# Performance work log

Hardware: AMD Instinct MI355X
Metric: run time of the kernel (lower is better)

The kernel has to match this reference:

```python
import jax, jax.numpy as jnp
import numpy as np

N_ENC, B, T, D_ENC = 3, 256, 168, 32
U, H, D_DEC, D_EXT = 256, 24, 1, 16


def _gru_cell(x, h, W, Uw, b):
    # Keras-style GRU cell: gates ordered [z, r, n]; h' = (1-z)*h + z*n
    u = Uw.shape[0]
    xg = x @ W + b            # [B, 3U]
    hg = h @ Uw               # [B, 3U]
    z = jax.nn.sigmoid(xg[:, :u] + hg[:, :u])
    r = jax.nn.sigmoid(xg[:, u:2 * u] + hg[:, u:2 * u])
    n = jnp.tanh(xg[:, 2 * u:] + r * hg[:, 2 * u:])
    return (1.0 - z) * h + z * n


def _run_gru(x, W, Uw, b):
    # x: [B, T, D] -> outputs [B, T, U], last state [B, U]
    h0 = jnp.zeros((x.shape[0], Uw.shape[0]), x.dtype)

    def step(h, xt):
        h2 = _gru_cell(xt, h, W, Uw, b)
        return h2, h2

    hT, ys = jax.lax.scan(step, h0, jnp.swapaxes(x, 0, 1))
    return jnp.swapaxes(ys, 0, 1), hT


def setup_inputs() -> dict:
    key = jax.random.key(0)
    ks = jax.random.split(key, 18)
    s = 0.05
    d_in_dec = N_ENC * U + D_DEC
    d_state = U + N_ENC * U
    return {
        "enc_inputs": jax.random.normal(ks[0], (N_ENC, B, T, D_ENC), jnp.float32),
        "dec_input": jax.random.normal(ks[1], (B, H, D_DEC), jnp.float32),
        "ext_feat": jax.random.normal(ks[2], (B, H, D_EXT), jnp.float32),
        "enc_W": jax.random.normal(ks[3], (N_ENC, D_ENC, 3 * U), jnp.float32) * s,
        "enc_U": jax.random.normal(ks[4], (N_ENC, U, 3 * U), jnp.float32) * s,
        "enc_b": jnp.zeros((N_ENC, 3 * U), jnp.float32),
        "att_W1": jax.random.normal(ks[5], (N_ENC, U, U), jnp.float32) * s,
        "att_W2": jax.random.normal(ks[6], (N_ENC, U, U), jnp.float32) * s,
        "att_v": jax.random.normal(ks[7], (N_ENC, U), jnp.float32) * s,
        "dec_W": jax.random.normal(ks[8], (d_in_dec, 3 * U), jnp.float32) * s,
        "dec_U": jax.random.normal(ks[9], (U, 3 * U), jnp.float32) * s,
        "dec_b": jnp.zeros((3 * U,), jnp.float32),
        "ext_W": jax.random.normal(ks[10], (D_EXT, U), jnp.float32) * s,
        "ext_b": jnp.zeros((U,), jnp.float32),
        "out1_W": jax.random.normal(ks[11], (d_state + U, U), jnp.float32) * s,
        "out1_b": jnp.zeros((U,), jnp.float32),
        "out2_W": jax.random.normal(ks[12], (U, D_DEC), jnp.float32) * s,
        "out2_b": jnp.zeros((D_DEC,), jnp.float32),
    }


def reference(enc_inputs, dec_input, ext_feat, enc_W, enc_U, enc_b,
              att_W1, att_W2, att_v, dec_W, dec_U, dec_b,
              ext_W, ext_b, out1_W, out1_b, out2_W, out2_b):
    b = dec_input.shape[0]
    horizon = dec_input.shape[1]

    # ---- encoders (vmapped GRU over the n_enc streams) ----
    enc_out, _ = jax.vmap(_run_gru)(enc_inputs, enc_W, enc_U, enc_b)  # [n,B,T,U]
    # Precompute Bahdanau keys once: W1 @ enc_outputs
    enc_proj = jnp.einsum('nbtu,nuv->nbtv', enc_out, att_W1)          # [n,B,T,U]

    h0 = jnp.zeros((b, U), dec_input.dtype)
    c0 = jnp.zeros((b, N_ENC * U), dec_input.dtype)

    def dec_step(carry, d_t):
        h, c = carry
        x_t = jnp.concatenate([c, d_t], axis=-1)                      # [B, n*U + D_dec]
        h = _gru_cell(x_t, h, dec_W, dec_U, dec_b)                    # [B, U]
        # Bahdanau attention per encoder, query = decoder state
        q = jnp.einsum('bu,nuv->nbv', h, att_W2)                      # [n,B,U]
        score = jnp.einsum('nbtv,nv->nbt',
                           jnp.tanh(enc_proj + q[:, :, None, :]), att_v)
        alpha = jax.nn.softmax(score, axis=-1)                        # [n,B,T]
        ctx = jnp.einsum('nbt,nbtu->nbu', alpha, enc_out)             # [n,B,U]
        c = jnp.transpose(ctx, (1, 0, 2)).reshape(b, N_ENC * U)
        return (h, c), h

    (h_last, c_last), _ = jax.lax.scan(dec_step, (h0, c0),
                                       jnp.swapaxes(dec_input, 0, 1))

    # ---- output head ----
    state = jnp.concatenate([h_last, c_last], axis=-1)                # [B, U + n*U]
    ed = jnp.broadcast_to(state[:, None, :], (b, horizon, state.shape[-1]))
    ext = jax.nn.relu(ext_feat @ ext_W + ext_b)                       # [B, H, U]
    x = jnp.concatenate([ed, ext], axis=-1)
    x = jax.nn.relu(x @ out1_W + out1_b)
    return x @ out2_W + out2_b                                        # [B, H, target_dim]
```

## Files before the change

kernel.cpp:

```cpp
#include <hip/hip_runtime.h>
#include <math.h>

typedef unsigned short u16;
typedef float f4v __attribute__((ext_vector_type(4)));
typedef _Float16 hfv8 __attribute__((ext_vector_type(8)));

#define MFMAH(a,b,c) __builtin_amdgcn_mfma_f32_16x16x32_f16((a),(b),(c),0,0,0)

__device__ __forceinline__ float bf2f(u16 x){
    unsigned int u = ((unsigned int)x) << 16;
    float f; __builtin_memcpy(&f, &u, 4); return f;
}
__device__ __forceinline__ u16 f2bf(float f){
    unsigned int u; __builtin_memcpy(&u, &f, 4);
    u += 0x7fffu + ((u >> 16) & 1u);
    return (u16)(u >> 16);
}
__device__ __forceinline__ u16 f2h(float f){
    _Float16 h = (_Float16)f;
    u16 b; __builtin_memcpy(&b, &h, 2); return b;
}
__device__ __forceinline__ float h2f(u16 b){
    _Float16 h; __builtin_memcpy(&h, &b, 2); return (float)h;
}
__device__ __forceinline__ float ldmix(const void* p, long i, int mode){
    if (mode) return ((const float*)p)[i];
    return bf2f(((const u16*)p)[i]);
}
__device__ __forceinline__ float frcp(float x){ return __builtin_amdgcn_rcpf(x); }
__device__ __forceinline__ float sigf(float x){ return frcp(1.0f+__expf(-x)); }
__device__ __forceinline__ float tanh_fast(float x){
    float e = __expf(2.0f*x);
    return 1.0f - 2.0f*frcp(1.0f+e);
}

#define BATCH 256
#define TLEN 168
#define HOR 24

#define OFF_FLAG 0ull
#define OFF_SENT 16ull
#define OFF_WF   256ull
#define OFF_UP   8721920ull
#define OFF_WP   9901568ull
#define OFF_DWP  10049024ull
#define OFF_DUP  11228672ull
#define OFF_H0   11621888ull
#define OFF_H1   11884032ull
#define OFF_C    12146176ull
#define OFF_W1P  12932608ull
#define OFF_SP   13719040ull
#define OFF_E    13981184ull
#define OFF_PACK0 OFF_E
#define OFF_PACK1 (OFF_E + 524288ull)
#define OFF_ENCOUT 17126912ull
#define OFF_PROJ 83187200ull
#define OFF_W2P  116217344ull
#define NEED_BYTES 149247488ull

#define W_ENCW 0
#define W_ENCU 73728
#define W_ENCB 663552
#define W_AW1  665856
#define W_AW2  862464
#define W_AV   1059072
#define W_DECW 1059840
#define W_DECU 1650432
#define W_DECB 1847040
#define W_EXTW 1847808
#define W_EXTB 1851904
#define W_O1W  1852160
#define W_O1B  2179840
#define W_O2W  2180096
#define W_O2B  2180352

__device__ const int c_wsz[15]  = {73728,589824,2304,196608,196608,768,590592,196608,768,4096,256,327680,256,256,1};
__device__ const int c_woff[15] = {W_ENCW,W_ENCU,W_ENCB,W_AW1,W_AW2,W_AV,W_DECW,W_DECU,W_DECB,W_EXTW,W_EXTB,W_O1W,W_O1B,W_O2W,W_O2B};

struct P15 { const void* p[15]; };

#define SENT_MAGIC 0x5AFE0000u
__device__ __forceinline__ void put_sent(char* ws, int idx){
    ((unsigned int*)(ws+OFF_SENT))[idx] = SENT_MAGIC | (unsigned int)idx;
}

__global__ __launch_bounds__(256) void k_probe(const u16* w16, char* ws)
{
    __shared__ float red[256];
    int tid = threadIdx.x;
    float mb = 0.0f;
    for (int i = tid; i < 2048; i += 256){
        float a = fabsf(bf2f(w16[i]));
        if (a > mb) mb = a;
    }
    red[tid] = mb;
    __syncthreads();
    if (tid == 0){
        for (int i = 1; i < 256; ++i) if (red[i] > mb) mb = red[i];
        *(int*)(ws+OFF_FLAG) = (mb > 1000.0f) ? 1 : 0;
        put_sent(ws, 0);
    }
}

__global__ __launch_bounds__(256) void k_convert(P15 in, char* ws)
{
    int mode = *(const int*)(ws+OFF_FLAG);
    float* F = (float*)(ws+OFF_WF);
    int y = blockIdx.y;
    int sz = c_wsz[y], off = c_woff[y];
    for (long i = (long)blockIdx.x*256 + threadIdx.x; i < sz; i += 256L*256L)
        F[off + i] = ldmix(in.p[y], i, mode);
    if (blockIdx.x==0 && blockIdx.y==0 && threadIdx.x==0) put_sent(ws, 1);
}

__global__ __launch_bounds__(64) void k_pack(char* ws)
{
    const float* F = (const float*)(ws+OFF_WF);
    int m = blockIdx.y;
    if (m >= 11){
        const float* s = F + W_AW2 + (m-11)*65536;
        u16* d = (u16*)(ws+OFF_W2P) + (m-11)*65536;
        int i = blockIdx.x*64 + threadIdx.x;
        if (i < 65536){
            int k = i>>8, u = i&255;
            d[(k>>1)*512 + u*2 + (k&1)] = f2h(s[i]);
        }
        return;
    }
    const float* src; u16* dst; int K, N; int duo = 0;
    switch (m) {
      case 0: case 1: case 2:
        src = F + W_ENCU + m*196608; dst = (u16*)(ws+OFF_UP) + m*196608; K=256; N=768; break;
      case 3: case 4: case 5:
        src = F + W_ENCW + (m-3)*24576; dst = (u16*)(ws+OFF_WP) + (m-3)*24576; K=32; N=768; break;
      case 6:
        src = F + W_DECW; dst = (u16*)(ws+OFF_DWP); K=768; N=768; break;
      case 7:
        src = F + W_DECU; dst = (u16*)(ws+OFF_DUP); K=256; N=768; break;
      default:
        src = F + W_AW1 + (m-8)*65536; dst = (u16*)(ws+OFF_W1P) + (m-8)*131072; K=256; N=256; duo=1; break;
    }
    int KT = K>>5, NT = N>>4;
    int tau = blockIdx.x;
    if (tau < KT*NT){
        int ct = tau / KT, kt = tau % KT;
        int l = threadIdx.x, q = l>>4, c = l&15;
        #pragma unroll
        for (int j = 0; j < 8; ++j){
            float v = src[(size_t)(kt*32 + q*8 + j)*N + ct*16 + c];
            u16 hi = f2h(v);
            size_t di = ((size_t)(ct*KT+kt)*64 + l)*8 + j;
            dst[di] = hi;
            if (duo) dst[65536 + di] = f2h(v - h2f(hi));
        }
    }
    if (blockIdx.x==0 && blockIdx.y==0 && threadIdx.x==0) put_sent(ws, 6);
}

__global__ __launch_bounds__(256) void k_init(char* ws)
{
    long idx = (long)blockIdx.x*256 + threadIdx.x;
    if (idx < 65536) ((float*)(ws+OFF_H0))[idx] = 0.0f;
    else if (idx < 262144) ((float*)(ws+OFF_C))[idx-65536] = 0.0f;
    else if (idx < 393216) ((int*)(ws+OFF_PACK0))[idx-262144] = 0;
}

__global__ __launch_bounds__(512, 2) void k_enc(const void* __restrict__ enc_in,
                                                char* __restrict__ ws,
                                                u16* __restrict__ enc_out)
{
    const float* __restrict__ F = (const float*)(ws+OFF_WF);
    int mode = *(const int*)(ws+OFF_FLAG);
    const int n  = blockIdx.y;
    const int b0 = blockIdx.x*16;
    const int tid = threadIdx.x;
    const int w = tid>>6, l = tid&63, quad = l>>4, c15 = l&15;

    __shared__ __align__(16) u16 hA[2][8][64][8];
    __shared__ __align__(16) u16 sx[2][64][8];
    __shared__ __align__(16) u16 nU[128][64][8];

    const u16* __restrict__ upn = (const u16*)(ws+OFF_UP) + n*196608;
    const u16* __restrict__ wpn = (const u16*)(ws+OFF_WP) + n*24576;

    {
        const uint4* s4 = (const uint4*)(upn + 131072);
        uint4* d4 = (uint4*)&nU[0][0][0];
        for (int i = tid; i < 8192; i += 512) d4[i] = s4[i];
    }
    {
        int* z0 = (int*)&hA[0][0][0][0];
        for (int i = tid; i < 2048; i += 512) z0[i]=0;
    }
    float h[8];
    #pragma unroll
    for (int i=0;i<8;++i) h[i]=0.0f;

    float bzr[2], brr[2], bnr[2];
    #pragma unroll
    for (int si=0;si<2;++si){
        int u = (w*2+si)*16 + c15;
        bzr[si] = F[W_ENCB + n*768 + u];
        brr[si] = F[W_ENCB + n*768 + 256 + u];
        bnr[si] = F[W_ENCB + n*768 + 512 + u];
    }

    hfv8 Bz[2][8], Br[2][8];
    #pragma unroll
    for (int si=0;si<2;++si){
        int ct = w*2+si;
        #pragma unroll
        for (int kt=0;kt<8;++kt){
            Bz[si][kt] = *(const hfv8*)(upn + ((size_t)(ct*8+kt)*64 + l)*8);
            Br[si][kt] = *(const hfv8*)(upn + ((size_t)((16+ct)*8+kt)*64 + l)*8);
        }
    }
    #pragma unroll
    for (int si=0;si<2;++si)
        #pragma unroll
        for (int kt=0;kt<8;++kt)
            asm volatile("" : "+v"(Bz[si][kt]), "+v"(Br[si][kt]));

    const int mm = tid>>5, kk2 = tid&31;
    sx[0][(kk2>>3)*16 + mm][kk2&7] =
        f2h(ldmix(enc_in, (((long)(n*BATCH + b0 + mm))*TLEN + 0)*32 + kk2, mode));
    __syncthreads();

    for (int t = 0; t < TLEN; ++t){
        int p = t & 1;

        int tt = (t+1 < TLEN) ? (t+1) : t;
        float xr = ldmix(enc_in, (((long)(n*BATCH + b0 + mm))*TLEN + tt)*32 + kk2, mode);

        hfv8 ah[8];
        #pragma unroll
        for (int kt=0; kt<8; ++kt)
            ah[kt] = *(const hfv8*)&hA[p][kt][l][0];
        hfv8 ax = *(const hfv8*)&sx[p][l][0];

        #pragma unroll
        for (int si=0; si<2; ++si){
            int ct = w*2 + si;
            f4v az  = {0.f,0.f,0.f,0.f};
            f4v ar  = {0.f,0.f,0.f,0.f};
            f4v anx = {0.f,0.f,0.f,0.f};
            f4v anh = {0.f,0.f,0.f,0.f};
            az  = MFMAH(ax, *(const hfv8*)(wpn + ((size_t)ct*64 + l)*8), az);
            ar  = MFMAH(ax, *(const hfv8*)(wpn + ((size_t)(16+ct)*64 + l)*8), ar);
            anx = MFMAH(ax, *(const hfv8*)(wpn + ((size_t)(32+ct)*64 + l)*8), anx);
            #pragma unroll
            for (int kt=0; kt<8; ++kt) az = MFMAH(ah[kt], Bz[si][kt], az);
            #pragma unroll
            for (int kt=0; kt<8; ++kt) ar = MFMAH(ah[kt], Br[si][kt], ar);
            #pragma unroll
            for (int kt=0; kt<8; ++kt)
                anh = MFMAH(ah[kt], *(const hfv8*)&nU[ct*8+kt][l][0], anh);
            int u = ct*16 + c15;
            #pragma unroll
            for (int j=0;j<4;++j){
                int m = quad*4 + j;
                float z = sigf(az[j] + bzr[si]);
                float r = sigf(ar[j] + brr[si]);
                float ng = tanh_fast(anx[j] + bnr[si] + r*anh[j]);
                float hn = (1.0f - z)*h[si*4+j] + z*ng;
                h[si*4+j] = hn;
                int kt = u>>5, q2 = (u>>3)&3, j2 = u&7;
                hA[1-p][kt][q2*16+m][j2] = f2h(hn);
            }
        }
        sx[1-p][(kk2>>3)*16 + mm][kk2&7] = f2h(xr);
        __syncthreads();
        {
            int c = tid & 31, m2 = tid >> 5;
            *reinterpret_cast<uint4*>(enc_out + (((long)(n*BATCH + b0 + m2))*TLEN + t)*256 + c*8) =
                *(const uint4*)&hA[1-p][c>>2][(c&3)*16 + m2][0];
        }
    }
    if (blockIdx.x==0 && blockIdx.y==0 && tid==0) put_sent(ws, 2);
}

__global__ __launch_bounds__(256) void k_projm(char* __restrict__ ws)
{
    const u16* __restrict__ enc16 = (const u16*)(ws+OFF_ENCOUT);
    const u16* __restrict__ w1p = (const u16*)(ws+OFF_W1P);
    u16* __restrict__ proj = (u16*)(ws+OFF_PROJ);
    const int n = blockIdx.y;
    const long r0 = (long)blockIdx.x*64;
    const int tid = threadIdx.x;
    const int w = tid>>6, l = tid&63, quad = l>>4, c15 = l&15;

    __shared__ __align__(16) u16 ob[64][264];

    const u16* erow = enc16 + ((long)n*43008 + r0 + w*16 + c15)*256;
    hfv8 a[8];
    #pragma unroll
    for (int kt=0; kt<8; ++kt)
        a[kt] = *(const hfv8*)(erow + kt*32 + quad*8);

    const u16* wb = w1p + (long)n*131072;
    #pragma unroll
    for (int ct=0; ct<16; ++ct){
        f4v acc = {0.f,0.f,0.f,0.f};
        #pragma unroll
        for (int kt=0; kt<8; ++kt)
            acc = MFMAH(a[kt], *(const hfv8*)(wb + ((size_t)(ct*8+kt)*64 + l)*8), acc);
        #pragma unroll
        for (int kt=0; kt<8; ++kt)
            acc = MFMAH(a[kt], *(const hfv8*)(wb + 65536 + ((size_t)(ct*8+kt)*64 + l)*8), acc);
        #pragma unroll
        for (int j=0;j<4;++j)
            ob[w*16 + quad*4 + j][ct*16 + c15] = f2h(acc[j]);
    }
    __syncthreads();
    for (int i = tid; i < 2048; i += 256){
        int r = i>>5, c = i&31;
        *reinterpret_cast<uint4*>(proj + ((long)n*43008 + r0 + r)*256 + c*8) =
            *(const uint4*)&ob[r][c*8];
    }
    if (blockIdx.x==0 && blockIdx.y==0 && tid==0) put_sent(ws, 3);
}

__global__ __launch_bounds__(192) void k_dec_gru(
    char* __restrict__ ws, const float* __restrict__ h_in, float* __restrict__ h_out,
    const u16* __restrict__ packC, u16* __restrict__ packN,
    const void* __restrict__ dec_in, int step)
{
    const float* __restrict__ F = (const float*)(ws+OFF_WF);
    int mode = *(const int*)(ws+OFF_FLAG);
    const u16* __restrict__ dwp = (const u16*)(ws+OFF_DWP);
    const u16* __restrict__ dup = (const u16*)(ws+OFF_DUP);
    const int bx = blockIdx.x;
    const int b0 = bx*16;
    const int us = blockIdx.y;
    const int u0 = us*16;
    const int tid = threadIdx.x;
    const int gate = tid>>6, l = tid&63, quad = l>>4, c15 = l&15;
    const int ct = gate*16 + us;

    __shared__ float gz[16][16], gr[16][16], gx[16][16], gh[16][16];

    const u16* pA = packC + (size_t)bx*16384;

    f4v accA  = {0.f,0.f,0.f,0.f};
    f4v accA2 = {0.f,0.f,0.f,0.f};
    f4v accB  = {0.f,0.f,0.f,0.f};
    f4v accB2 = {0.f,0.f,0.f,0.f};

    #pragma unroll
    for (int kg = 0; kg < 32; ++kg){
        hfv8 av = *(const hfv8*)(pA + ((size_t)kg*64 + l)*8);
        const u16* bp = (kg < 24) ? dwp + ((size_t)(ct*24 + kg)*64 + l)*8
                                  : dup + ((size_t)(ct*8  + (kg-24))*64 + l)*8;
        hfv8 bv = *(const hfv8*)bp;
        if (gate == 2 && kg >= 24){
            if (kg & 1) accB2 = MFMAH(av, bv, accB2);
            else        accB  = MFMAH(av, bv, accB);
        } else {
            if (kg & 1) accA2 = MFMAH(av, bv, accA2);
            else        accA  = MFMAH(av, bv, accA);
        }
    }
    accA = accA + accA2;
    accB = accB + accB2;

    #pragma unroll
    for (int j=0;j<4;++j){
        int m = quad*4 + j;
        if (gate == 0) gz[m][c15] = accA[j];
        else if (gate == 1) gr[m][c15] = accA[j];
        else { gx[m][c15] = accA[j]; gh[m][c15] = accB[j]; }
    }
    __syncthreads();
    for (int e = tid; e < 256; e += 192){
        int m = e>>4, j = e&15;
        int u = u0 + j;
        int b = b0 + m;
        float db = ldmix(dec_in, (long)b*HOR + step, mode);
        float sz = gz[m][j] + db*F[W_DECW + 768*768 + u]       + F[W_DECB + u];
        float sr = gr[m][j] + db*F[W_DECW + 768*768 + 256 + u] + F[W_DECB + 256 + u];
        float sn = gx[m][j] + db*F[W_DECW + 768*768 + 512 + u] + F[W_DECB + 512 + u];
        float z = sigf(sz);
        float r = sigf(sr);
        float ng = tanh_fast(sn + r*gh[m][j]);
        float hn = (1.0f - z)*h_in[(long)b*256 + u] + z*ng;
        h_out[(long)b*256 + u] = hn;
        int kk = u & 31;
        int kg = 24 + (u >> 5);
        packN[(((size_t)bx*32 + kg)*64 + (kk>>3)*16 + m)*8 + (kk&7)] = f2h(hn);
    }
}

__global__ __launch_bounds__(256) void k_attn(char* __restrict__ ws,
                                              const float* __restrict__ hvec,
                                              u16* __restrict__ packN)
{
    const float* __restrict__ F = (const float*)(ws+OFF_WF);
    const u16* __restrict__ proj = (const u16*)(ws+OFF_PROJ);
    const u16* __restrict__ enc16 = (const u16*)(ws+OFF_ENCOUT);
    float* __restrict__ C = (float*)(ws+OFF_C);
    const int b = blockIdx.x, n = blockIdx.y;
    const int tid = threadIdx.x;
    const int w = tid>>6, l = tid&63;

    __shared__ float ps[TLEN][65];
    __shared__ float sc[TLEN];
    __shared__ float red[8];
    __shared__ float hrow[256];
    __shared__ float sq[256];

    hrow[tid] = hvec[(long)b*256 + tid];
    __syncthreads();
    {
        const u16* W2p = (const u16*)(ws+OFF_W2P) + n*65536;
        float q0=0.f,q1=0.f,q2=0.f,q3=0.f;
        #pragma unroll 4
        for (int k2 = 0; k2 < 128; k2 += 2){
            unsigned va = *(const unsigned*)(W2p + (size_t)k2*512 + tid*2);
            unsigned vb = *(const unsigned*)(W2p + (size_t)(k2+1)*512 + tid*2);
            q0 += hrow[2*k2  ]*h2f((u16)(va & 0xffffu));
            q1 += hrow[2*k2+1]*h2f((u16)(va >> 16));
            q2 += hrow[2*k2+2]*h2f((u16)(vb & 0xffffu));
            q3 += hrow[2*k2+3]*h2f((u16)(vb >> 16));
        }
        sq[tid] = (q0+q1)+(q2+q3);
    }
    __syncthreads();

    float qv[4], vv[4];
    #pragma unroll
    for (int c4 = 0; c4 < 4; ++c4){
        qv[c4] = sq[c4*64 + l];
        vv[c4] = F[W_AV + n*256 + c4*64 + l];
    }
    long base = ((long)n*43008 + (long)b*TLEN)*256;
    const u16* pb = proj + base;

    for (int i = 0; i < 42; ++i){
        int t = w*42 + i;
        float s = 0.0f;
        #pragma unroll
        for (int c4 = 0; c4 < 4; ++c4){
            float pv = h2f(pb[(long)t*256 + c4*64 + l]);
            s += vv[c4]*tanh_fast(pv + qv[c4]);
        }
        ps[t][l] = s;
    }
    __syncthreads();

    float sval = 0.0f;
    if (tid < TLEN){
        float s0=0.f,s1=0.f,s2=0.f,s3=0.f,s4=0.f,s5=0.f,s6=0.f,s7=0.f;
        #pragma unroll
        for (int j = 0; j < 64; j += 8){
            s0 += ps[tid][j];   s1 += ps[tid][j+1];
            s2 += ps[tid][j+2]; s3 += ps[tid][j+3];
            s4 += ps[tid][j+4]; s5 += ps[tid][j+5];
            s6 += ps[tid][j+6]; s7 += ps[tid][j+7];
        }
        sval = ((s0+s1)+(s2+s3)) + ((s4+s5)+(s6+s7));
    }

    float m = (tid < TLEN) ? sval : -1e30f;
    #pragma unroll
    for (int off = 32; off > 0; off >>= 1) m = fmaxf(m, __shfl_xor(m, off, 64));
    if (l == 0) red[w] = m;
    __syncthreads();
    float mx = fmaxf(fmaxf(red[0],red[1]), fmaxf(red[2],red[3]));

    float ex = 0.0f;
    if (tid < TLEN){ ex = __expf(sval - mx); sc[tid] = ex; }
    float su = ex;
    #pragma unroll
    for (int off = 32; off > 0; off >>= 1) su += __shfl_xor(su, off, 64);
    if (l == 0) red[4+w] = su;
    __syncthreads();
    float inv = frcp((red[4]+red[5]) + (red[6]+red[7]));

    const u16* eb = enc16 + base;
    float a0=0.f,a1=0.f,a2=0.f,a3=0.f,a4=0.f,a5=0.f,a6=0.f,a7=0.f;
    for (int t = 0; t < TLEN; t += 8){
        a0 += sc[t  ]*h2f(eb[(long)(t  )*256 + tid]);
        a1 += sc[t+1]*h2f(eb[(long)(t+1)*256 + tid]);
        a2 += sc[t+2]*h2f(eb[(long)(t+2)*256 + tid]);
        a3 += sc[t+3]*h2f(eb[(long)(t+3)*256 + tid]);
        a4 += sc[t+4]*h2f(eb[(long)(t+4)*256 + tid]);
        a5 += sc[t+5]*h2f(eb[(long)(t+5)*256 + tid]);
        a6 += sc[t+6]*h2f(eb[(long)(t+6)*256 + tid]);
        a7 += sc[t+7]*h2f(eb[(long)(t+7)*256 + tid]);
    }
    float cv = (((a0+a1)+(a2+a3)) + ((a4+a5)+(a6+a7)))*inv;
    C[(long)b*768 + n*256 + tid] = cv;
    {
        int kg = n*8 + (tid>>5), kk = tid&31;
        packN[(((size_t)(b>>4)*32 + kg)*64 + (kk>>3)*16 + (b&15))*8 + (kk&7)] = f2h(cv);
    }
    if (b==0 && n==0 && tid==0) put_sent(ws, 4);
}

__global__ __launch_bounds__(256) void k_head1(char* ws, const float* h_last)
{
    const float* F = (const float*)(ws+OFF_WF);
    const float* C = (const float*)(ws+OFF_C);
    float* SP = (float*)(ws+OFF_SP);
    const int b0 = blockIdx.x*8;
    const int tid = threadIdx.x;

    __shared__ float A[8][1024];
    for (int i = tid; i < 8192; i += 256){
        int r = i >> 10, k = i & 1023;
        A[r][k] = (k < 256) ? h_last[(long)(b0+r)*256 + k]
                            : C[(long)(b0+r)*768 + (k-256)];
    }
    __syncthreads();

    const float* W = F + W_O1W;
    float acc[8];
    float bc = F[W_O1B + tid];
    #pragma unroll
    for (int r = 0; r < 8; ++r) acc[r] = bc;
    for (int k = 0; k < 1024; ++k){
        float w = W[k*256 + tid];
        #pragma unroll
        for (int r = 0; r < 8; ++r) acc[r] += A[r][k]*w;
    }
    for (int r = 0; r < 8; ++r)
        SP[(long)(b0+r)*256 + tid] = acc[r];
}

__global__ __launch_bounds__(256) void k_ext(const void* ext_feat, char* ws)
{
    const float* F = (const float*)(ws+OFF_WF);
    u16* E = (u16*)(ws+OFF_E);
    int mode = *(const int*)(ws+OFF_FLAG);
    const int r0 = blockIdx.x*64;
    const int tid = threadIdx.x;
    __shared__ float ef[64][16];
    for (int i = tid; i < 1024; i += 256)
        ef[i>>4][i&15] = ldmix(ext_feat, (long)(r0 + (i>>4))*16 + (i&15), mode);
    float wreg[16];
    #pragma unroll
    for (int k = 0; k < 16; ++k) wreg[k] = F[W_EXTW + k*256 + tid];
    float bb = F[W_EXTB + tid];
    __syncthreads();
    for (int r = 0; r < 64; ++r){
        float a = bb;
        #pragma unroll
        for (int k = 0; k < 16; ++k) a += ef[r][k]*wreg[k];
        E[(long)(r0+r)*256 + tid] = f2bf((a > 0.0f) ? a : 0.0f);
    }
}

__global__ __launch_bounds__(256) void k_head2(char* ws, void* out)
{
    const float* F = (const float*)(ws+OFF_WF);
    const u16* E = (const u16*)(ws+OFF_E);
    const float* SP = (const float*)(ws+OFF_SP);
    int mode = *(const int*)(ws+OFF_FLAG);
    const int r0 = blockIdx.x*16;
    const int tid = threadIdx.x;
    const int w = tid>>6, l = tid&63;

    __shared__ float A[16][256];
    __shared__ float x1[16][257];
    for (int i = tid; i < 4096; i += 256)
        A[i>>8][i&255] = bf2f(E[(long)r0*256 + i]);
    __syncthreads();

    const float* W = F + W_O1W + 1024*256;
    float acc[16];
    float bc = F[W_O1B + tid];
    #pragma unroll
    for (int r = 0; r < 16; ++r) acc[r] = 0.0f;
    for (int k = 0; k < 256; ++k){
        float wv = W[k*256 + tid];
        #pragma unroll
        for (int r = 0; r < 16; ++r) acc[r] += A[r][k]*wv;
    }
    for (int r = 0; r < 16; ++r){
        int g = r0 + r;
        int b = g / HOR;
        float v = acc[r] + SP[(long)b*256 + tid] + bc;
        x1[r][tid] = (v > 0.0f) ? v : 0.0f;
    }
    __syncthreads();

    float w2v[4];
    #pragma unroll
    for (int c4 = 0; c4 < 4; ++c4) w2v[c4] = F[W_O2W + c4*64 + l];
    float b2 = F[W_O2B];
    #pragma unroll
    for (int rr = 0; rr < 4; ++rr){
        int m = w*4 + rr;
        float s = 0.0f;
        #pragma unroll
        for (int c4 = 0; c4 < 4; ++c4) s += x1[m][c4*64 + l]*w2v[c4];
        for (int off = 32; off > 0; off >>= 1) s += __shfl_xor(s, off, 64);
        if (l == 0){
            float val = s + b2;
            long g = r0 + m;
            if (mode == 0) ((u16*)out)[g] = f2bf(val);
            else           ((float*)out)[g] = val;
        }
    }
    if (blockIdx.x==0 && tid==0) put_sent(ws, 5);
}

__global__ __launch_bounds__(64) void MTANet_7593502179851_kernel(char* ws, void* out)
{
    if (threadIdx.x == 0){
        const unsigned int* sent = (const unsigned int*)(ws+OFF_SENT);
        int mode = *(const int*)(ws+OFF_FLAG);
        for (int i = 0; i < 7; ++i){
            if (sent[i] != (SENT_MAGIC | (unsigned int)i)){
                float code = 400.0f + 10.0f*(float)i;
                if (mode == 0) ((u16*)out)[0] = f2bf(code);
                else           ((float*)out)[0] = code;
                break;
            }
        }
    }
}

__global__ __launch_bounds__(64) void k_diag(void* out, float code)
{
    if (threadIdx.x == 0){
        ((u16*)out)[0] = f2bf(code);
        ((float*)out)[1] = code;
    }
}

extern "C" void kernel_launch(void* const* d_in, const int* in_sizes, int n_in,
                              void* d_out, int out_size, void* d_ws, size_t ws_size,
                              hipStream_t stream)
{
    char* ws = (char*)d_ws;

    static const int exp_sizes[18] = {
        4128768, 6144, 98304, 73728, 589824, 2304, 196608, 196608, 768,
        590592, 196608, 768, 4096, 256, 327680, 256, 256, 1 };
    int bad_i = -1;
    if (n_in != 18) bad_i = 99;
    else for (int i = 0; i < 18; ++i)
        if (in_sizes[i] != exp_sizes[i]){ bad_i = i; break; }
    if (bad_i >= 0){
        k_diag<<<dim3(1), dim3(64), 0, stream>>>(d_out, 900.0f + (float)bad_i);
        return;
    }
    if (ws_size < (size_t)NEED_BYTES){
        k_diag<<<dim3(1), dim3(64), 0, stream>>>(d_out, 600.0f);
        return;
    }

    P15 wp;
    for (int i = 0; i < 15; ++i) wp.p[i] = d_in[3+i];

    hipError_t le[12];
    for (int i = 0; i < 12; ++i) le[i] = hipSuccess;
    (void)hipGetLastError();
    #define CHK(slot) { hipError_t e_ = hipGetLastError(); if (e_ != hipSuccess && le[slot] == hipSuccess) le[slot] = e_; }

    k_probe<<<dim3(1), dim3(256), 0, stream>>>((const u16*)d_in[3], ws);       CHK(0)
    k_convert<<<dim3(256,15), dim3(256), 0, stream>>>(wp, ws);                 CHK(1)
    k_pack<<<dim3(1152,14), dim3(64), 0, stream>>>(ws);                        CHK(2)
    k_init<<<dim3(1536), dim3(256), 0, stream>>>(ws);                          CHK(3)
    k_enc<<<dim3(16,3), dim3(512), 0, stream>>>(d_in[0], ws, (u16*)(ws+OFF_ENCOUT)); CHK(4)
    k_projm<<<dim3(672,3), dim3(256), 0, stream>>>(ws);                        CHK(5)

    float* hbuf0 = (float*)(ws+OFF_H0);
    float* hbuf1 = (float*)(ws+OFF_H1);
    u16* pk0 = (u16*)(ws+OFF_PACK0);
    u16* pk1 = (u16*)(ws+OFF_PACK1);
    float* h_last = hbuf0;
    for (int s = 0; s < HOR; ++s){
        float* h_in  = (s & 1) ? hbuf1 : hbuf0;
        float* h_out = (s & 1) ? hbuf0 : hbuf1;
        u16* pc = (s & 1) ? pk1 : pk0;
        u16* pn = (s & 1) ? pk0 : pk1;
        k_dec_gru<<<dim3(16,16), dim3(192), 0, stream>>>(ws, h_in, h_out, pc, pn, d_in[1], s); CHK(6)
        k_attn<<<dim3(256,3), dim3(256), 0, stream>>>(ws, h_out, pn);           CHK(7)
        h_last = h_out;
    }
    k_head1<<<dim3(32), dim3(256), 0, stream>>>(ws, h_last);                   CHK(8)
    k_ext<<<dim3(96), dim3(256), 0, stream>>>(d_in[2], ws);                    CHK(9)
    k_head2<<<dim3(384), dim3(256), 0, stream>>>(ws, d_out);                   CHK(10)
    MTANet_7593502179851_kernel<<<dim3(1), dim3(64), 0, stream>>>(ws, d_out);
    #undef CHK

    for (int i = 0; i < 12; ++i){
        if (le[i] != hipSuccess){
            k_diag<<<dim3(1), dim3(64), 0, stream>>>(d_out, 800.0f + (float)i);
            break;
        }
    }
}
```

Before: 1.648 ms.

## Fuse decoder GRU and attention steps into one persistent kernel with group barriers

Replaces the 48 per-step launches (GRU kernel plus attention kernel for each of 24 horizon steps) with a single persistent kernel of 256 blocks. Each group of 16 blocks synchronizes through global atomic counters, used as spin barriers, after the GRU update and after attention. Attention now loops over the three encoders inside a block and splits the query and context reductions across 512 threads. The W2 packed buffer moves to a smaller offset. This removes launch overhead, at the cost of depending on all 256 blocks being co-resident and on spin-wait correctness.

```diff
diff --git a/kernel.cpp b/kernel.cpp
--- a/kernel.cpp
+++ b/kernel.cpp
@@ -40,6 +40,7 @@
 
 #define OFF_FLAG 0ull
 #define OFF_SENT 16ull
+#define OFF_CNT  128ull
 #define OFF_WF   256ull
 #define OFF_UP   8721920ull
 #define OFF_WP   9901568ull
@@ -53,9 +54,9 @@
 #define OFF_E    13981184ull
 #define OFF_PACK0 OFF_E
 #define OFF_PACK1 (OFF_E + 524288ull)
+#define OFF_W2P   (OFF_E + 1048576ull)
 #define OFF_ENCOUT 17126912ull
 #define OFF_PROJ 83187200ull
-#define OFF_W2P  116217344ull
 #define NEED_BYTES 149247488ull
 
 #define W_ENCW 0
@@ -163,6 +164,7 @@
     if (idx < 65536) ((float*)(ws+OFF_H0))[idx] = 0.0f;
     else if (idx < 262144) ((float*)(ws+OFF_C))[idx-65536] = 0.0f;
     else if (idx < 393216) ((int*)(ws+OFF_PACK0))[idx-262144] = 0;
+    if (idx < 32) ((unsigned*)(ws+OFF_CNT))[idx] = 0u;
 }
 
 __global__ __launch_bounds__(512, 2) void k_enc(const void* __restrict__ enc_in,
@@ -228,7 +230,6 @@
 
     for (int t = 0; t < TLEN; ++t){
         int p = t & 1;
-
         int tt = (t+1 < TLEN) ? (t+1) : t;
         float xr = ldmix(enc_in, (((long)(n*BATCH + b0 + mm))*TLEN + tt)*32 + kk2, mode);
 
@@ -320,181 +321,219 @@
     if (blockIdx.x==0 && blockIdx.y==0 && tid==0) put_sent(ws, 3);
 }
 
-__global__ __launch_bounds__(192) void k_dec_gru(
-    char* __restrict__ ws, const float* __restrict__ h_in, float* __restrict__ h_out,
-    const u16* __restrict__ packC, u16* __restrict__ packN,
-    const void* __restrict__ dec_in, int step)
+__global__ __launch_bounds__(512, 2) void k_dec_all(
+    char* __restrict__ ws, const void* __restrict__ dec_in,
+    u16* __restrict__ pk0, u16* __restrict__ pk1,
+    float* __restrict__ h0, float* __restrict__ h1)
 {
     const float* __restrict__ F = (const float*)(ws+OFF_WF);
-    int mode = *(const int*)(ws+OFF_FLAG);
     const u16* __restrict__ dwp = (const u16*)(ws+OFF_DWP);
     const u16* __restrict__ dup = (const u16*)(ws+OFF_DUP);
-    const int bx = blockIdx.x;
-    const int b0 = bx*16;
-    const int us = blockIdx.y;
-    const int u0 = us*16;
-    const int tid = threadIdx.x;
-    const int gate = tid>>6, l = tid&63, quad = l>>4, c15 = l&15;
-    const int ct = gate*16 + us;
-
-    __shared__ float gz[16][16], gr[16][16], gx[16][16], gh[16][16];
-
-    const u16* pA = packC + (size_t)bx*16384;
-
-    f4v accA  = {0.f,0.f,0.f,0.f};
-    f4v accA2 = {0.f,0.f,0.f,0.f};
-    f4v accB  = {0.f,0.f,0.f,0.f};
-    f4v accB2 = {0.f,0.f,0.f,0.f};
-
-    #pragma unroll
-    for (int kg = 0; kg < 32; ++kg){
-        hfv8 av = *(const hfv8*)(pA + ((size_t)kg*64 + l)*8);
-        const u16* bp = (kg < 24) ? dwp + ((size_t)(ct*24 + kg)*64 + l)*8
-                                  : dup + ((size_t)(ct*8  + (kg-24))*64 + l)*8;
-        hfv8 bv = *(const hfv8*)bp;
-        if (gate == 2 && kg >= 24){
-            if (kg & 1) accB2 = MFMAH(av, bv, accB2);
-            else        accB  = MFMAH(av, bv, accB);
-        } else {
-            if (kg & 1) accA2 = MFMAH(av, bv, accA2);
-            else        accA  = MFMAH(av, bv, accA);
-        }
-    }
-    accA = accA + accA2;
-    accB = accB + accB2;
-
-    #pragma unroll
-    for (int j=0;j<4;++j){
-        int m = quad*4 + j;
-        if (gate == 0) gz[m][c15] = accA[j];
-        else if (gate == 1) gr[m][c15] = accA[j];
-        else { gx[m][c15] = accA[j]; gh[m][c15] = accB[j]; }
-    }
-    __syncthreads();
-    for (int e = tid; e < 256; e += 192){
-        int m = e>>4, j = e&15;
-        int u = u0 + j;
-        int b = b0 + m;
-        float db = ldmix(dec_in, (long)b*HOR + step, mode);
-        float sz = gz[m][j] + db*F[W_DECW + 768*768 + u]       + F[W_DECB + u];
-        float sr = gr[m][j] + db*F[W_DECW + 768*768 + 256 + u] + F[W_DECB + 256 + u];
-        float sn = gx[m][j] + db*F[W_DECW + 768*768 + 512 + u] + F[W_DECB + 512 + u];
-        float z = sigf(sz);
-        float r = sigf(sr);
-        float ng = tanh_fast(sn + r*gh[m][j]);
-        float hn = (1.0f - z)*h_in[(long)b*256 + u] + z*ng;
-        h_out[(long)b*256 + u] = hn;
-        int kk = u & 31;
-        int kg = 24 + (u >> 5);
-        packN[(((size_t)bx*32 + kg)*64 + (kk>>3)*16 + m)*8 + (kk&7)] = f2h(hn);
-    }
-}
-
-__global__ __launch_bounds__(256) void k_attn(char* __restrict__ ws,
-                                              const float* __restrict__ hvec,
-                                              u16* __restrict__ packN)
-{
-    const float* __restrict__ F = (const float*)(ws+OFF_WF);
     const u16* __restrict__ proj = (const u16*)(ws+OFF_PROJ);
     const u16* __restrict__ enc16 = (const u16*)(ws+OFF_ENCOUT);
     float* __restrict__ C = (float*)(ws+OFF_C);
-    const int b = blockIdx.x, n = blockIdx.y;
+    int mode = *(const int*)(ws+OFF_FLAG);
+
+    const int blk = blockIdx.x;
+    const int g = blk >> 4;
+    const int r = blk & 15;
     const int tid = threadIdx.x;
     const int w = tid>>6, l = tid&63;
-
+    const int b = g*16 + r;
+
+    unsigned* cnt = (unsigned*)(ws+OFF_CNT) + (size_t)g*2;
+
+    __shared__ float gz[16][16], gr[16][16], gx[16][16], gh[16][16];
     __shared__ float ps[TLEN][65];
     __shared__ float sc[TLEN];
-    __shared__ float red[8];
+    __shared__ float red[16];
     __shared__ float hrow[256];
     __shared__ float sq[256];
-
-    hrow[tid] = hvec[(long)b*256 + tid];
-    __syncthreads();
-    {
-        const u16* W2p = (const u16*)(ws+OFF_W2P) + n*65536;
-        float q0=0.f,q1=0.f,q2=0.f,q3=0.f;
-        #pragma unroll 4
-        for (int k2 = 0; k2 < 128; k2 += 2){
-            unsigned va = *(const unsigned*)(W2p + (size_t)k2*512 + tid*2);
-            unsigned vb = *(const unsigned*)(W2p + (size_t)(k2+1)*512 + tid*2);
-            q0 += hrow[2*k2  ]*h2f((u16)(va & 0xffffu));
-            q1 += hrow[2*k2+1]*h2f((u16)(va >> 16));
-            q2 += hrow[2*k2+2]*h2f((u16)(vb & 0xffffu));
-            q3 += hrow[2*k2+3]*h2f((u16)(vb >> 16));
-        }
-        sq[tid] = (q0+q1)+(q2+q3);
-    }
-    __syncthreads();
-
-    float qv[4], vv[4];
-    #pragma unroll
-    for (int c4 = 0; c4 < 4; ++c4){
-        qv[c4] = sq[c4*64 + l];
-        vv[c4] = F[W_AV + n*256 + c4*64 + l];
-    }
-    long base = ((long)n*43008 + (long)b*TLEN)*256;
-    const u16* pb = proj + base;
-
-    for (int i = 0; i < 42; ++i){
-        int t = w*42 + i;
-        float s = 0.0f;
-        #pragma unroll
-        for (int c4 = 0; c4 < 4; ++c4){
-            float pv = h2f(pb[(long)t*256 + c4*64 + l]);
-            s += vv[c4]*tanh_fast(pv + qv[c4]);
-        }
-        ps[t][l] = s;
-    }
-    __syncthreads();
-
-    float sval = 0.0f;
-    if (tid < TLEN){
-        float s0=0.f,s1=0.f,s2=0.f,s3=0.f,s4=0.f,s5=0.f,s6=0.f,s7=0.f;
-        #pragma unroll
-        for (int j = 0; j < 64; j += 8){
-            s0 += ps[tid][j];   s1 += ps[tid][j+1];
-            s2 += ps[tid][j+2]; s3 += ps[tid][j+3];
-            s4 += ps[tid][j+4]; s5 += ps[tid][j+5];
-            s6 += ps[tid][j+6]; s7 += ps[tid][j+7];
-        }
-        sval = ((s0+s1)+(s2+s3)) + ((s4+s5)+(s6+s7));
-    }
-
-    float m = (tid < TLEN) ? sval : -1e30f;
-    #pragma unroll
-    for (int off = 32; off > 0; off >>= 1) m = fmaxf(m, __shfl_xor(m, off, 64));
-    if (l == 0) red[w] = m;
-    __syncthreads();
-    float mx = fmaxf(fmaxf(red[0],red[1]), fmaxf(red[2],red[3]));
-
-    float ex = 0.0f;
-    if (tid < TLEN){ ex = __expf(sval - mx); sc[tid] = ex; }
-    float su = ex;
-    #pragma unroll
-    for (int off = 32; off > 0; off >>= 1) su += __shfl_xor(su, off, 64);
-    if (l == 0) red[4+w] = su;
-    __syncthreads();
-    float inv = frcp((red[4]+red[5]) + (red[6]+red[7]));
-
-    const u16* eb = enc16 + base;
-    float a0=0.f,a1=0.f,a2=0.f,a3=0.f,a4=0.f,a5=0.f,a6=0.f,a7=0.f;
-    for (int t = 0; t < TLEN; t += 8){
-        a0 += sc[t  ]*h2f(eb[(long)(t  )*256 + tid]);
-        a1 += sc[t+1]*h2f(eb[(long)(t+1)*256 + tid]);
-        a2 += sc[t+2]*h2f(eb[(long)(t+2)*256 + tid]);
-        a3 += sc[t+3]*h2f(eb[(long)(t+3)*256 + tid]);
-        a4 += sc[t+4]*h2f(eb[(long)(t+4)*256 + tid]);
-        a5 += sc[t+5]*h2f(eb[(long)(t+5)*256 + tid]);
-        a6 += sc[t+6]*h2f(eb[(long)(t+6)*256 + tid]);
-        a7 += sc[t+7]*h2f(eb[(long)(t+7)*256 + tid]);
-    }
-    float cv = (((a0+a1)+(a2+a3)) + ((a4+a5)+(a6+a7)))*inv;
-    C[(long)b*768 + n*256 + tid] = cv;
-    {
-        int kg = n*8 + (tid>>5), kk = tid&31;
-        packN[(((size_t)(b>>4)*32 + kg)*64 + (kk>>3)*16 + (b&15))*8 + (kk&7)] = f2h(cv);
-    }
-    if (b==0 && n==0 && tid==0) put_sent(ws, 4);
+    __shared__ float sqp[2][256];
+    __shared__ float ctxp[2][256];
+
+    for (int s = 0; s < HOR; ++s){
+        const u16* packC = (s & 1) ? pk1 : pk0;
+        u16* packN      = (s & 1) ? pk0 : pk1;
+        const float* h_in  = (s & 1) ? h1 : h0;
+        float* h_out       = (s & 1) ? h0 : h1;
+
+        if (tid < 192){
+            const int gate = tid>>6, quad = l>>4, c15 = l&15;
+            const int ct = gate*16 + r;
+            const u16* pA = packC + (size_t)g*16384;
+
+            f4v accA  = {0.f,0.f,0.f,0.f};
+            f4v accA2 = {0.f,0.f,0.f,0.f};
+            f4v accB  = {0.f,0.f,0.f,0.f};
+            f4v accB2 = {0.f,0.f,0.f,0.f};
+            #pragma unroll
+            for (int kg = 0; kg < 32; ++kg){
+                hfv8 av = *(const hfv8*)(pA + ((size_t)kg*64 + l)*8);
+                const u16* bp = (kg < 24) ? dwp + ((size_t)(ct*24 + kg)*64 + l)*8
+                                          : dup + ((size_t)(ct*8  + (kg-24))*64 + l)*8;
+                hfv8 bv = *(const hfv8*)bp;
+                if (gate == 2 && kg >= 24){
+                    if (kg & 1) accB2 = MFMAH(av, bv, accB2);
+                    else        accB  = MFMAH(av, bv, accB);
+                } else {
+                    if (kg & 1) accA2 = MFMAH(av, bv, accA2);
+                    else        accA  = MFMAH(av, bv, accA);
+                }
+            }
+            accA = accA + accA2;
+            accB = accB + accB2;
+            #pragma unroll
+            for (int j=0;j<4;++j){
+                int m = quad*4 + j;
+                if (gate == 0) gz[m][c15] = accA[j];
+                else if (gate == 1) gr[m][c15] = accA[j];
+                else { gx[m][c15] = accA[j]; gh[m][c15] = accB[j]; }
+            }
+        }
+        __syncthreads();
+        if (tid < 256){
+            int m = tid>>4, j = tid&15;
+            int u = r*16 + j;
+            int bb = g*16 + m;
+            float db = ldmix(dec_in, (long)bb*HOR + s, mode);
+            float sz = gz[m][j] + db*F[W_DECW + 768*768 + u]       + F[W_DECB + u];
+            float sr = gr[m][j] + db*F[W_DECW + 768*768 + 256 + u] + F[W_DECB + 256 + u];
+            float sn = gx[m][j] + db*F[W_DECW + 768*768 + 512 + u] + F[W_DECB + 512 + u];
+            float z = sigf(sz);
+            float rr2 = sigf(sr);
+            float ng = tanh_fast(sn + rr2*gh[m][j]);
+            float hn = (1.0f - z)*h_in[(long)bb*256 + u] + z*ng;
+            h_out[(long)bb*256 + u] = hn;
+            int kk = u & 31;
+            int kg = 24 + (u >> 5);
+            packN[(((size_t)g*32 + kg)*64 + (kk>>3)*16 + m)*8 + (kk&7)] = f2h(hn);
+        }
+
+        __syncthreads();
+        if (tid == 0){
+            __threadfence();
+            atomicAdd(cnt+0, 1u);
+            unsigned tgt = 16u*(unsigned)(s+1);
+            int sp = 0;
+            while (atomicAdd(cnt+0, 0u) < tgt && sp < 4000000) ++sp;
+        }
+        __syncthreads();
+        __threadfence();
+
+        if (tid < 256) hrow[tid] = h_out[(long)b*256 + tid];
+        __syncthreads();
+
+        for (int n = 0; n < 3; ++n){
+            {
+                const u16* W2p = (const u16*)(ws+OFF_W2P) + n*65536;
+                int uu = tid & 255, half = tid >> 8;
+                float q0=0.f,q1=0.f,q2=0.f,q3=0.f;
+                #pragma unroll 4
+                for (int k2 = half*64; k2 < half*64+64; k2 += 2){
+                    unsigned va = *(const unsigned*)(W2p + (size_t)k2*512 + uu*2);
+                    unsigned vb = *(const unsigned*)(W2p + (size_t)(k2+1)*512 + uu*2);
+                    q0 += hrow[2*k2  ]*h2f((u16)(va & 0xffffu));
+                    q1 += hrow[2*k2+1]*h2f((u16)(va >> 16));
+                    q2 += hrow[2*k2+2]*h2f((u16)(vb & 0xffffu));
+                    q3 += hrow[2*k2+3]*h2f((u16)(vb >> 16));
+                }
+                sqp[half][uu] = (q0+q1)+(q2+q3);
+            }
+            __syncthreads();
+            if (tid < 256) sq[tid] = sqp[0][tid] + sqp[1][tid];
+            __syncthreads();
+
+            float qv[4], vv[4];
+            #pragma unroll
+            for (int c4 = 0; c4 < 4; ++c4){
+                qv[c4] = sq[c4*64 + l];
+                vv[c4] = F[W_AV + n*256 + c4*64 + l];
+            }
+            long base = ((long)n*43008 + (long)b*TLEN)*256;
+            const u16* pb = proj + base;
+
+            for (int i = 0; i < 21; ++i){
+                int t = w*21 + i;
+                float sacc = 0.0f;
+                #pragma unroll
+                for (int c4 = 0; c4 < 4; ++c4){
+                    float pv = h2f(pb[(long)t*256 + c4*64 + l]);
+                    sacc += vv[c4]*tanh_fast(pv + qv[c4]);
+                }
+                ps[t][l] = sacc;
+            }
+            __syncthreads();
+
+            float sval = 0.0f;
+            if (tid < TLEN){
+                float s0=0.f,s1=0.f,s2=0.f,s3=0.f,s4=0.f,s5=0.f,s6=0.f,s7=0.f;
+                #pragma unroll
+                for (int j = 0; j < 64; j += 8){
+                    s0 += ps[tid][j];   s1 += ps[tid][j+1];
+                    s2 += ps[tid][j+2]; s3 += ps[tid][j+3];
+                    s4 += ps[tid][j+4]; s5 += ps[tid][j+5];
+                    s6 += ps[tid][j+6]; s7 += ps[tid][j+7];
+                }
+                sval = ((s0+s1)+(s2+s3)) + ((s4+s5)+(s6+s7));
+            }
+            float mval = (tid < TLEN) ? sval : -1e30f;
+            #pragma unroll
+            for (int off = 32; off > 0; off >>= 1) mval = fmaxf(mval, __shfl_xor(mval, off, 64));
+            if (l == 0) red[w] = mval;
+            __syncthreads();
+            float mx = fmaxf(fmaxf(fmaxf(red[0],red[1]), fmaxf(red[2],red[3])),
+                             fmaxf(fmaxf(red[4],red[5]), fmaxf(red[6],red[7])));
+            float ex = 0.0f;
+            if (tid < TLEN){ ex = __expf(sval - mx); sc[tid] = ex; }
+            float su = ex;
+            #pragma unroll
+            for (int off = 32; off > 0; off >>= 1) su += __shfl_xor(su, off, 64);
+            if (l == 0) red[8+w] = su;
+            __syncthreads();
+            float inv = frcp(((red[8]+red[9])+(red[10]+red[11])) +
+                             ((red[12]+red[13])+(red[14]+red[15])));
+
+            {
+                const u16* eb = enc16 + base;
+                int uu = tid & 255, half = tid >> 8;
+                int t0 = half ? 88 : 0;
+                int t1 = half ? 168 : 88;
+                float a0=0.f,a1=0.f,a2=0.f,a3=0.f,a4=0.f,a5=0.f,a6=0.f,a7=0.f;
+                for (int t = t0; t < t1; t += 8){
+                    a0 += sc[t  ]*h2f(eb[(long)(t  )*256 + uu]);
+                    a1 += sc[t+1]*h2f(eb[(long)(t+1)*256 + uu]);
+                    a2 += sc[t+2]*h2f(eb[(long)(t+2)*256 + uu]);
+                    a3 += sc[t+3]*h2f(eb[(long)(t+3)*256 + uu]);
+                    a4 += sc[t+4]*h2f(eb[(long)(t+4)*256 + uu]);
+                    a5 += sc[t+5]*h2f(eb[(long)(t+5)*256 + uu]);
+                    a6 += sc[t+6]*h2f(eb[(long)(t+6)*256 + uu]);
+                    a7 += sc[t+7]*h2f(eb[(long)(t+7)*256 + uu]);
+                }
+                ctxp[half][uu] = (((a0+a1)+(a2+a3)) + ((a4+a5)+(a6+a7)));
+            }
+            __syncthreads();
+            if (tid < 256){
+                float cv = (ctxp[0][tid] + ctxp[1][tid])*inv;
+                int kg = n*8 + (tid>>5), kk = tid&31;
+                packN[(((size_t)g*32 + kg)*64 + (kk>>3)*16 + r)*8 + (kk&7)] = f2h(cv);
+                if (s == HOR-1) C[(long)b*768 + n*256 + tid] = cv;
+            }
+            __syncthreads();
+        }
+
+        __syncthreads();
+        if (tid == 0){
+            __threadfence();
+            atomicAdd(cnt+1, 1u);
+            unsigned tgt = 16u*(unsigned)(s+1);
+            int sp = 0;
+            while (atomicAdd(cnt+1, 0u) < tgt && sp < 4000000) ++sp;
+        }
+        __syncthreads();
+        __threadfence();
+    }
+    if (blk == 0 && tid == 0) put_sent(ws, 4);
 }
 
 __global__ __launch_bounds__(256) void k_head1(char* ws, const float* h_last)
@@ -670,17 +709,9 @@
     float* hbuf1 = (float*)(ws+OFF_H1);
     u16* pk0 = (u16*)(ws+OFF_PACK0);
     u16* pk1 = (u16*)(ws+OFF_PACK1);
-    float* h_last = hbuf0;
-    for (int s = 0; s < HOR; ++s){
-        float* h_in  = (s & 1) ? hbuf1 : hbuf0;
-        float* h_out = (s & 1) ? hbuf0 : hbuf1;
-        u16* pc = (s & 1) ? pk1 : pk0;
-        u16* pn = (s & 1) ? pk0 : pk1;
-        k_dec_gru<<<dim3(16,16), dim3(192), 0, stream>>>(ws, h_in, h_out, pc, pn, d_in[1], s); CHK(6)
-        k_attn<<<dim3(256,3), dim3(256), 0, stream>>>(ws, h_out, pn);           CHK(7)
-        h_last = h_out;
-    }
-    k_head1<<<dim3(32), dim3(256), 0, stream>>>(ws, h_last);                   CHK(8)
+    k_dec_all<<<dim3(256), dim3(512), 0, stream>>>(ws, d_in[1], pk0, pk1, hbuf0, hbuf1); CHK(6)
+
+    k_head1<<<dim3(32), dim3(256), 0, stream>>>(ws, hbuf0);                    CHK(8)
     k_ext<<<dim3(96), dim3(256), 0, stream>>>(d_in[2], ws);                    CHK(9)
     k_head2<<<dim3(384), dim3(256), 0, stream>>>(ws, d_out);                   CHK(10)
     MTANet_7593502179851_kernel<<<dim3(1), dim3(64), 0, stream>>>(ws, d_out);
```

Result: slower. 4.422 ms (+168.3%).
